# Performance work log

Measured on AMD Instinct MI355X. Metric: run time of the kernel, lower is better.

## Reference

```python
import jax, jax.numpy as jnp
import numpy as np
import math

D_MODEL = 1024
N_HEADS = 16
D_HEAD = D_MODEL // N_HEADS
D_FF = 4096
BATCH = 2
SEQ = 2048
EPS = 1e-5


def _rmsnorm(x, w):
    rms = jnp.sqrt(jnp.mean(x * x, axis=-1, keepdims=True) + EPS)
    return (x / rms) * w


def _gelu_erf(x):
    # matches 0.5 * x * (1 + erf(x / sqrt(2)))
    return 0.5 * x * (1.0 + jax.lax.erf(x / jnp.sqrt(jnp.asarray(2.0, x.dtype))))


def setup_inputs() -> dict:
    key = jax.random.key(0)
    ks = jax.random.split(key, 6)
    scale = 0.02
    x = jax.random.normal(ks[0], (BATCH, SEQ, D_MODEL), dtype=jnp.float32)
    w_qkv = jax.random.normal(ks[1], (3 * D_MODEL, D_MODEL), dtype=jnp.float32) * scale
    w_o = jax.random.normal(ks[2], (D_MODEL, D_MODEL), dtype=jnp.float32) * scale
    ln1_w = jnp.ones((D_MODEL,), dtype=jnp.float32)
    ln2_w = jnp.ones((D_MODEL,), dtype=jnp.float32)
    w1 = jax.random.normal(ks[3], (D_FF, D_MODEL), dtype=jnp.float32) * scale
    w2 = jax.random.normal(ks[4], (D_MODEL, D_FF), dtype=jnp.float32) * scale
    return {"x": x, "w_qkv": w_qkv, "w_o": w_o, "ln1_w": ln1_w,
            "ln2_w": ln2_w, "w1": w1, "w2": w2}


def reference(x, w_qkv, w_o, ln1_w, ln2_w, w1, w2):
    B, S, D = x.shape
    # --- attention sublayer (pre-norm) ---
    h = _rmsnorm(x, ln1_w)
    qkv = jnp.einsum('bsd,ed->bse', h, w_qkv)            # (B,S,3*D)
    qkv = qkv.reshape(B, S, 3, N_HEADS, D_HEAD)
    q, k, v = jnp.moveaxis(qkv, 2, 0)                    # each (B,S,H,dh)
    q = q.transpose(0, 2, 1, 3)                          # (B,H,S,dh)
    k = k.transpose(0, 2, 1, 3)
    v = v.transpose(0, 2, 1, 3)
    scores = jnp.einsum('bhqd,bhkd->bhqk', q, k) / math.sqrt(D_HEAD)
    causal = jnp.tril(jnp.ones((S, S), dtype=bool))      # True = keep
    scores = jnp.where(causal, scores, jnp.asarray(-jnp.inf, scores.dtype))
    attn = jax.nn.softmax(scores, axis=-1)
    ctx = jnp.einsum('bhqk,bhkd->bhqd', attn, v)         # (B,H,S,dh)
    ctx = ctx.transpose(0, 2, 1, 3).reshape(B, S, D)
    attn_out = jnp.einsum('bsd,ed->bse', ctx, w_o)
    first_sum = x + attn_out
    # --- FFN sublayer (pre-norm) ---
    h2 = _rmsnorm(first_sum, ln2_w)
    ff = jnp.einsum('bsf,df->bsd', _gelu_erf(jnp.einsum('bsd,fd->bsf', h2, w1)), w2)
    return first_sum + ff
```

## Files before the change

kernel.cpp:

```cpp
#include <hip/hip_runtime.h>

typedef unsigned short u16;
typedef unsigned int u32;
typedef __attribute__((ext_vector_type(8))) short short8;
typedef __attribute__((ext_vector_type(4))) float f32x4;

#define AS1 __attribute__((address_space(1)))
#define AS3 __attribute__((address_space(3)))

__device__ __forceinline__ u16 f2bf(float f) {
  union { float f; unsigned u; } v; v.f = f;
  return (u16)((v.u + 0x7fffu + ((v.u >> 16) & 1u)) >> 16);
}
__device__ __forceinline__ u32 pack2bf(float a, float b) {
  return (u32)f2bf(a) | ((u32)f2bf(b) << 16);
}
__device__ __forceinline__ float bf2f(u16 h) {
  union { u32 u; float f; } v; v.u = ((u32)h) << 16; return v.f;
}
__device__ __forceinline__ u32 permpack(float a, float b) {
  union { float f; u32 u; } ua, ub; ua.f = a; ub.f = b;
  return __builtin_amdgcn_perm(ub.u, ua.u, 0x07060302u);
}


__global__ __launch_bounds__(256)
void packb_kernel(const float* __restrict__ wqkv, const float* __restrict__ wo,
                  const float* __restrict__ w1, const float* __restrict__ w2,
                  u16* __restrict__ oqkv, u16* __restrict__ oo,
                  u16* __restrict__ o1, u16* __restrict__ o2) {
  __shared__ u16 Ls[128][40];
  const int b = blockIdx.x, t = threadIdx.x;
  const float* W; u16* O; int nb, kb, KB; float scale = 1.0f;
  if (b < 768)       { W = wqkv; O = oqkv; KB = 32;  int i2 = b;        nb = i2 >> 5; kb = i2 & 31;
                       if (nb >= 8 && nb < 16) scale = 0.125f; }
  else if (b < 1024) { W = wo;   O = oo;   KB = 32;  int i2 = b - 768;  nb = i2 >> 5; kb = i2 & 31; }
  else if (b < 2048) { W = w1;   O = o1;   KB = 32;  int i2 = b - 1024; nb = i2 >> 5; kb = i2 & 31; }
  else               { W = w2;   O = o2;   KB = 128; int i2 = b - 2048; nb = i2 >> 7; kb = i2 & 127; }
  const int K = KB * 32;
  {
    const int r = t >> 1, c0 = (t & 1) * 16;
    const float* src = W + (size_t)(nb * 128 + r) * K + kb * 32 + c0;
#pragma unroll
    for (int e = 0; e < 16; ++e) Ls[r][c0 + e] = f2bf(src[e] * scale);
  }
  __syncthreads();
  const int f = t >> 5, l0 = (t & 31) * 2;
  u16* dst = O + ((size_t)(nb * KB + kb) * 8 + f) * 512 + (size_t)l0 * 8;
  short8 v0, v1;
#pragma unroll
  for (int e = 0; e < 8; ++e) v0[e] = (short)Ls[f * 16 + (l0 & 15)][(l0 >> 4) * 8 + e];
  const int l1 = l0 + 1;
#pragma unroll
  for (int e = 0; e < 8; ++e) v1[e] = (short)Ls[f * 16 + (l1 & 15)][(l1 >> 4) * 8 + e];
  *(short8*)dst = v0;
  *(short8*)(dst + 8) = v1;
}

__global__ void rmsnorm_kernel(const float* __restrict__ x, const float* __restrict__ w,
                               u16* __restrict__ out) {
  const int row = blockIdx.x, tid = threadIdx.x;
  const float4 v = ((const float4*)(x + (size_t)row * 1024))[tid];
  float ss = v.x * v.x + v.y * v.y + v.z * v.z + v.w * v.w;
#pragma unroll
  for (int off = 32; off > 0; off >>= 1) ss += __shfl_xor(ss, off);
  __shared__ float red[4];
  if ((tid & 63) == 0) red[tid >> 6] = ss;
  __syncthreads();
  float tot = red[0] + red[1] + red[2] + red[3];
  float scale = 1.0f / sqrtf(tot * (1.0f / 1024.0f) + 1e-5f);
  const float4 wv = ((const float4*)w)[tid];
  const int kb = tid >> 3, quadp = (tid >> 1) & 3, e0 = (tid & 1) * 4;
  const int mb = row >> 7, i_o = (row >> 4) & 7, l16_o = row & 15;
  size_t off = (((size_t)mb * 32 + kb) * 8 + i_o) * 512 + (quadp * 16 + l16_o) * 8 + e0;
  u32 lo = pack2bf(v.x * scale * wv.x, v.y * scale * wv.y);
  u32 hi = pack2bf(v.z * scale * wv.z, v.w * scale * wv.w);
  *(uint2*)(out + off) = make_uint2(lo, hi);
}

template <int EPI>
__global__ __launch_bounds__(256, 3)
void gemm_pp(const u16* __restrict__ Ap, const u16* __restrict__ Bp,
             const float* __restrict__ RES, void* __restrict__ OUT,
             int M, int N, int K, int KS) {
  __shared__ __align__(16) u16 As[2][4096];
  const int tid = threadIdx.x;
  const int wave = tid >> 6, lane = tid & 63;
  const int quad = lane >> 4, l16 = lane & 15;
  int bx = blockIdx.x, by = blockIdx.y;
  const int gx = gridDim.x, gy = gridDim.y;
  if (((gx & 1) | (gy & 3)) == 0) {
    const int lin = blockIdx.x + gx * blockIdx.y;
    const int xcd = lin & 7, j = lin >> 3;
    const int rw = gx >> 1;
    bx = (xcd & 1) * rw + j % rw;
    by = (xcd >> 1) * (gy >> 2) + j / rw;
  }
  const int wm = (wave >> 1) * 64, wn = (wave & 1) * 64;
  const int KB = K >> 5;
  f32x4 acc[4][4] = {};

  const int kb0 = (blockIdx.z * KS) >> 5;
  const int nit = KS >> 5;
  const u16* Ag = Ap + ((size_t)by * KB + kb0) * 4096 + wave * 1024 + lane * 8;
  const u16* Bw = Bp + (((size_t)bx * KB + kb0) * 8 + (wn >> 4)) * 512 + (size_t)lane * 8;

  auto stage = [&](int it, int pp) {
    const u16* s = Ag + (size_t)it * 4096;
    u16* d = &As[pp][wave * 1024];
    __builtin_amdgcn_global_load_lds((AS1 void*)s, (AS3 void*)d, 16, 0, 0);
    __builtin_amdgcn_global_load_lds((AS1 void*)(s + 512), (AS3 void*)(d + 512), 16, 0, 0);
  };

  stage(0, 0);
  short8 bfr[4];
#pragma unroll
  for (int j = 0; j < 4; ++j) bfr[j] = *(const short8*)(Bw + j * 512);
  int p = 0;
  const int abase = (wm >> 4) * 512;
  for (int it = 0; it < nit - 1; ++it) {
    __syncthreads();
    stage(it + 1, p ^ 1);
    short8 bn[4];
    {
      const u16* bp = Bw + (size_t)(it + 1) * 4096;
#pragma unroll
      for (int j = 0; j < 4; ++j) bn[j] = *(const short8*)(bp + j * 512);
    }
    short8 af[4];
#pragma unroll
    for (int i = 0; i < 4; ++i)
      af[i] = *(const short8*)(&As[p][abase + i * 512 + lane * 8]);
#pragma unroll
    for (int i = 0; i < 4; ++i)
#pragma unroll
      for (int j = 0; j < 4; ++j)
        acc[i][j] = __builtin_amdgcn_mfma_f32_16x16x32_bf16(af[i], bfr[j], acc[i][j], 0, 0, 0);
#pragma unroll
    for (int j = 0; j < 4; ++j) bfr[j] = bn[j];
    p ^= 1;
  }
  {
    __syncthreads();
    short8 af[4];
#pragma unroll
    for (int i = 0; i < 4; ++i)
      af[i] = *(const short8*)(&As[p][abase + i * 512 + lane * 8]);
#pragma unroll
    for (int i = 0; i < 4; ++i)
#pragma unroll
      for (int j = 0; j < 4; ++j)
        acc[i][j] = __builtin_amdgcn_mfma_f32_16x16x32_bf16(af[i], bfr[j], acc[i][j], 0, 0, 0);
  }

  const int m0 = by * 128, n0 = bx * 128;
  const size_t zoff = (size_t)blockIdx.z * M * N;
#pragma unroll
  for (int i = 0; i < 4; ++i) {
#pragma unroll
    for (int j = 0; j < 4; ++j) {
#pragma unroll
      for (int r = 0; r < 4; ++r) {
        int row = m0 + wm + i * 16 + quad * 4 + r;
        int col = n0 + wn + j * 16 + l16;
        size_t idx = (size_t)row * N + col;
        float v = acc[i][j][r];
        if constexpr (EPI == 0) {
          ((u16*)OUT)[idx] = f2bf(v);
        } else if constexpr (EPI == 1) {
          ((float*)OUT)[idx] = RES[idx] + v;
        } else if constexpr (EPI == 2) {
          float g = 0.5f * v * (1.0f + erff(v * 0.70710678118654752f));
          const int kb_o = col >> 5, quadp = (col >> 3) & 3, e = col & 7;
          const int mb_o = row >> 7, i_o = (row >> 4) & 7, l16_o = row & 15;
          size_t off = (((size_t)mb_o * (N >> 5) + kb_o) * 8 + i_o) * 512
                       + (quadp * 16 + l16_o) * 8 + e;
          ((u16*)OUT)[off] = f2bf(g);
        } else {
          ((u16*)OUT)[zoff + idx] = f2bf(v);
        }
      }
    }
  }
}

__global__ void reduce4_kernel(const float* __restrict__ fs,
                               const u16* __restrict__ P,
                               float* __restrict__ out, size_t n) {
  size_t i = ((size_t)blockIdx.x * 256 + threadIdx.x) * 4;
  float4 a = *(const float4*)(fs + i);
  float s[4] = {a.x, a.y, a.z, a.w};
#pragma unroll
  for (int z = 0; z < 4; ++z) {
    ushort4 q = *(const ushort4*)(P + z * n + i);
    s[0] += bf2f(q.x); s[1] += bf2f(q.y); s[2] += bf2f(q.z); s[3] += bf2f(q.w);
  }
  *(float4*)(out + i) = make_float4(s[0], s[1], s[2], s[3]);
}

__global__ __launch_bounds__(256)
void packkv_kernel(const u16* __restrict__ qkv, u16* __restrict__ Kp,
                   u16* __restrict__ Vp) {
  __shared__ __align__(16) u16 Ks[32][72];
  __shared__ __align__(16) u16 Vs[32][72];
  const int kt = blockIdx.x, h = blockIdx.y, b = blockIdx.z;
  const int tid = threadIdx.x;
  const int key0 = kt * 32;
  {
    const size_t g = (size_t)b * 2048 * 3072 + (size_t)(key0 + (tid >> 3)) * 3072
                     + h * 64 + (tid & 7) * 8;
    *(short8*)(&Ks[tid >> 3][(tid & 7) * 8]) = *(const short8*)(qkv + g + 1024);
    *(short8*)(&Vs[tid >> 3][(tid & 7) * 8]) = *(const short8*)(qkv + g + 2048);
  }
  __syncthreads();
  const int wave = tid >> 6, lane = tid & 63;
  const int quad = lane >> 4, l16 = lane & 15;
  const int permrow = 8 * (l16 >> 2) + (l16 & 3);
  const size_t obase = ((size_t)((b * 16 + h) * 64 + kt)) * 2048 + tid * 8;
  {
    int row = permrow + (wave >> 1) * 4;
    int col = quad * 8 + (wave & 1) * 32;
    *(short8*)(Kp + obase) = *(const short8*)(&Ks[row][col]);
  }
  {
    short8 v;
    int col = wave * 16 + l16;
#pragma unroll
    for (int j = 0; j < 8; ++j) v[j] = (short)Vs[quad * 8 + j][col];
    *(short8*)(Vp + obase) = v;
  }
}

struct AttnState {
  f32x4 o0, o1, o2, o3;
  float ls;
};

template <bool MASKED>
__device__ __forceinline__ void attn_tile(
    AttnState& st, const u16* kp, const u16* vp, int key0, int q_abs, int quad,
    short8 qf0, short8 qf1) {
  short8 kf00 = *(const short8*)kp;
  short8 kf01 = *(const short8*)(kp + 512);
  short8 kf10 = *(const short8*)(kp + 1024);
  short8 kf11 = *(const short8*)(kp + 1536);
  short8 vf0 = *(const short8*)vp;
  short8 vf1 = *(const short8*)(vp + 512);
  short8 vf2 = *(const short8*)(vp + 1024);
  short8 vf3 = *(const short8*)(vp + 1536);

  f32x4 s0 = {}, s1 = {};
  s0 = __builtin_amdgcn_mfma_f32_16x16x32_bf16(kf00, qf0, s0, 0, 0, 0);
  s0 = __builtin_amdgcn_mfma_f32_16x16x32_bf16(kf01, qf1, s0, 0, 0, 0);
  s1 = __builtin_amdgcn_mfma_f32_16x16x32_bf16(kf10, qf0, s1, 0, 0, 0);
  s1 = __builtin_amdgcn_mfma_f32_16x16x32_bf16(kf11, qf1, s1, 0, 0, 0);

  float p[8];
#pragma unroll
  for (int r = 0; r < 4; ++r) {
    p[r]     = __expf(s0[r]);
    p[4 + r] = __expf(s1[r]);
  }
  if constexpr (MASKED) {
    const int kb = key0 + 8 * quad;
#pragma unroll
    for (int r = 0; r < 4; ++r) {
      if (kb + r > q_abs)     p[r] = 0.f;
      if (kb + 4 + r > q_abs) p[4 + r] = 0.f;
    }
  }
  st.ls += ((p[0] + p[1]) + (p[2] + p[3])) + ((p[4] + p[5]) + (p[6] + p[7]));

  union { u32 u[4]; short8 s; } pu;
  pu.u[0] = permpack(p[0], p[1]);
  pu.u[1] = permpack(p[2], p[3]);
  pu.u[2] = permpack(p[4], p[5]);
  pu.u[3] = permpack(p[6], p[7]);

  st.o0 = __builtin_amdgcn_mfma_f32_16x16x32_bf16(vf0, pu.s, st.o0, 0, 0, 0);
  st.o1 = __builtin_amdgcn_mfma_f32_16x16x32_bf16(vf1, pu.s, st.o1, 0, 0, 0);
  st.o2 = __builtin_amdgcn_mfma_f32_16x16x32_bf16(vf2, pu.s, st.o2, 0, 0, 0);
  st.o3 = __builtin_amdgcn_mfma_f32_16x16x32_bf16(vf3, pu.s, st.o3, 0, 0, 0);
}

__global__ __launch_bounds__(256)
void attn_kernel(const u16* __restrict__ qkv, const u16* __restrict__ Kpack,
                 const u16* __restrict__ Vpack, u16* __restrict__ ctx) {
  const int bx = blockIdx.x, by = blockIdx.y, bz = blockIdx.z;
  const int h = by, b = bz;
  const int qt = ((by >> 3) & 1) ? (31 - bx) : bx;
  const int tid = threadIdx.x, wave = tid >> 6, lane = tid & 63;
  const int quad = lane >> 4, l16 = lane & 15;
  const int q0 = qt * 64;
  const int qrow = q0 + wave * 16;
  const int q_abs = qrow + l16;
  const size_t base = (size_t)b * 2048 * 3072;
  const size_t headoff = (size_t)((b * 16 + h) * 64) * 2048;
  const u16* Kb = Kpack + headoff + lane * 8;
  const u16* Vb = Vpack + headoff + lane * 8;

  short8 qf0, qf1;
  {
    const u16* qp = qkv + base + (size_t)q_abs * 3072 + h * 64 + quad * 8;
    qf0 = *(const short8*)qp;
    qf1 = *(const short8*)(qp + 32);
  }
  AttnState st;
  st.o0 = f32x4{}; st.o1 = f32x4{}; st.o2 = f32x4{}; st.o3 = f32x4{};
  st.ls = 0.f;

  const int nfull = qrow >> 5;
  for (int kt = 0; kt < nfull; ++kt)
    attn_tile<false>(st, Kb + kt * 2048, Vb + kt * 2048, kt * 32, q_abs, quad, qf0, qf1);
  attn_tile<true>(st, Kb + nfull * 2048, Vb + nfull * 2048, nfull * 32, q_abs, quad, qf0, qf1);

  float ls = st.ls;
  ls += __shfl_xor(ls, 16);
  ls += __shfl_xor(ls, 32);
  float inv = 1.0f / ls;

  const int rgl = b * 2048 + q_abs;
  const int mb = rgl >> 7, i_o = (rgl >> 4) & 7;
  f32x4 o[4] = {st.o0, st.o1, st.o2, st.o3};
#pragma unroll
  for (int c = 0; c < 4; ++c) {
    const int c0 = h * 64 + c * 16 + quad * 4;
    const int kb = c0 >> 5, quadp = (c0 >> 3) & 3, e0 = c0 & 7;
    size_t off = (((size_t)mb * 32 + kb) * 8 + i_o) * 512 + (quadp * 16 + l16) * 8 + e0;
    u32 lo = pack2bf(o[c][0] * inv, o[c][1] * inv);
    u32 hi = pack2bf(o[c][2] * inv, o[c][3] * inv);
    *(uint2*)(ctx + off) = make_uint2(lo, hi);
  }
}

extern "C" void kernel_launch(void* const* d_in, const int* in_sizes, int n_in,
                              void* d_out, int out_size, void* d_ws, size_t ws_size,
                              hipStream_t stream) {
  const float* x     = (const float*)d_in[0];
  const float* w_qkv = (const float*)d_in[1];
  const float* w_o   = (const float*)d_in[2];
  const float* ln1   = (const float*)d_in[3];
  const float* ln2   = (const float*)d_in[4];
  const float* w1    = (const float*)d_in[5];
  const float* w2    = (const float*)d_in[6];
  float* out = (float*)d_out;

  char* p = (char*)d_ws;
  u16* wqkv_b = (u16*)p; p += (size_t)3072 * 1024 * 2;
  u16* wo_b   = (u16*)p; p += (size_t)1024 * 1024 * 2;
  u16* w1_b   = (u16*)p; p += (size_t)4096 * 1024 * 2;
  u16* w2_b   = (u16*)p; p += (size_t)1024 * 4096 * 2;
  u16* h_b    = (u16*)p; p += (size_t)4096 * 1024 * 2;
  u16* qkv_b  = (u16*)p;
  u16* g_b    = qkv_b;
  p += (size_t)4096 * 3072 * 2;
  u16* ctx_b  = (u16*)p; p += (size_t)4096 * 1024 * 2;
  float* fs   = (float*)p; p += (size_t)4096 * 1024 * 4;
  u16* kp_b   = (u16*)fs;
  u16* vp_b   = (u16*)fs + (size_t)4 * 1024 * 1024;
  u16* Pbuf = (u16*)p;
  const size_t need = (size_t)(p - (char*)d_ws) + (size_t)4 * 4096 * 1024 * 2;
  const bool splitk = ws_size >= need;

  packb_kernel<<<3072, 256, 0, stream>>>(w_qkv, w_o, w1, w2,
                                         wqkv_b, wo_b, w1_b, w2_b);

  rmsnorm_kernel<<<4096, 256, 0, stream>>>(x, ln1, h_b);
  gemm_pp<0><<<dim3(24, 32, 1), 256, 0, stream>>>(h_b, wqkv_b, nullptr, qkv_b, 4096, 3072, 1024, 1024);
  packkv_kernel<<<dim3(64, 16, 2), 256, 0, stream>>>(qkv_b, kp_b, vp_b);
  attn_kernel<<<dim3(32, 16, 2), 256, 0, stream>>>(qkv_b, kp_b, vp_b, ctx_b);
  gemm_pp<1><<<dim3(8, 32, 1), 256, 0, stream>>>(ctx_b, wo_b, x, fs, 4096, 1024, 1024, 1024);
  rmsnorm_kernel<<<4096, 256, 0, stream>>>(fs, ln2, h_b);
  gemm_pp<2><<<dim3(32, 32, 1), 256, 0, stream>>>(h_b, w1_b, nullptr, g_b, 4096, 4096, 1024, 1024);
  if (splitk) {
    gemm_pp<3><<<dim3(8, 32, 4), 256, 0, stream>>>(g_b, w2_b, nullptr, Pbuf, 4096, 1024, 4096, 1024);
    reduce4_kernel<<<4096, 256, 0, stream>>>(fs, Pbuf, out, (size_t)4096 * 1024);
  } else {
    gemm_pp<1><<<dim3(8, 32, 1), 256, 0, stream>>>(g_b, w2_b, fs, out, 4096, 1024, 4096, 4096);
  }
}
```

Baseline: 320.0 us.

## Split-K the output projection, unroll GEMM K-loop by two, vectorize weight packing

Several separate changes. The attention output projection GEMM now runs split-K across 4 slices into bf16 partial buffers, with a reduce kernel that adds the residual x, so a 256-block grid becomes 1024 blocks. The GEMM main loop is unrolled by two with fixed ping-pong B register sets, and launch bounds go from 3 to 4 blocks per CU. The weight packing kernel uses vectorized float4 loads and uint4 LDS stores. The risks are an extra reduce pass, partial sums rounded to bf16, and more register pressure under the higher occupancy target. The unrolled loop also assumes an even, nonzero number of K iterations.

```diff
diff --git a/kernel.cpp b/kernel.cpp
--- a/kernel.cpp
+++ b/kernel.cpp
@@ -29,7 +29,7 @@
                   const float* __restrict__ w1, const float* __restrict__ w2,
                   u16* __restrict__ oqkv, u16* __restrict__ oo,
                   u16* __restrict__ o1, u16* __restrict__ o2) {
-  __shared__ u16 Ls[128][40];
+  __shared__ __align__(16) u16 Ls[128][40];
   const int b = blockIdx.x, t = threadIdx.x;
   const float* W; u16* O; int nb, kb, KB; float scale = 1.0f;
   if (b < 768)       { W = wqkv; O = oqkv; KB = 32;  int i2 = b;        nb = i2 >> 5; kb = i2 & 31;
@@ -41,20 +41,25 @@
   {
     const int r = t >> 1, c0 = (t & 1) * 16;
     const float* src = W + (size_t)(nb * 128 + r) * K + kb * 32 + c0;
-#pragma unroll
-    for (int e = 0; e < 16; ++e) Ls[r][c0 + e] = f2bf(src[e] * scale);
-  }
-  __syncthreads();
-  const int f = t >> 5, l0 = (t & 31) * 2;
+    float4 v0 = *(const float4*)(src);
+    float4 v1 = *(const float4*)(src + 4);
+    float4 v2 = *(const float4*)(src + 8);
+    float4 v3 = *(const float4*)(src + 12);
+    uint4 a, c;
+    a.x = pack2bf(v0.x * scale, v0.y * scale); a.y = pack2bf(v0.z * scale, v0.w * scale);
+    a.z = pack2bf(v1.x * scale, v1.y * scale); a.w = pack2bf(v1.z * scale, v1.w * scale);
+    c.x = pack2bf(v2.x * scale, v2.y * scale); c.y = pack2bf(v2.z * scale, v2.w * scale);
+    c.z = pack2bf(v3.x * scale, v3.y * scale); c.w = pack2bf(v3.z * scale, v3.w * scale);
+    *(uint4*)&Ls[r][c0] = a;
+    *(uint4*)&Ls[r][c0 + 8] = c;
+  }
+  __syncthreads();
+  const int f = t >> 5, l0 = (t & 31) * 2, l1 = l0 + 1;
   u16* dst = O + ((size_t)(nb * KB + kb) * 8 + f) * 512 + (size_t)l0 * 8;
-  short8 v0, v1;
-#pragma unroll
-  for (int e = 0; e < 8; ++e) v0[e] = (short)Ls[f * 16 + (l0 & 15)][(l0 >> 4) * 8 + e];
-  const int l1 = l0 + 1;
-#pragma unroll
-  for (int e = 0; e < 8; ++e) v1[e] = (short)Ls[f * 16 + (l1 & 15)][(l1 >> 4) * 8 + e];
-  *(short8*)dst = v0;
-  *(short8*)(dst + 8) = v1;
+  uint4 w0 = *(const uint4*)&Ls[f * 16 + (l0 & 15)][(l0 >> 4) * 8];
+  uint4 w1v = *(const uint4*)&Ls[f * 16 + (l1 & 15)][(l1 >> 4) * 8];
+  *(uint4*)dst = w0;
+  *(uint4*)(dst + 8) = w1v;
 }
 
 __global__ void rmsnorm_kernel(const float* __restrict__ x, const float* __restrict__ w,
@@ -79,7 +84,7 @@
 }
 
 template <int EPI>
-__global__ __launch_bounds__(256, 3)
+__global__ __launch_bounds__(256, 4)
 void gemm_pp(const u16* __restrict__ Ap, const u16* __restrict__ Bp,
              const float* __restrict__ RES, void* __restrict__ OUT,
              int M, int N, int K, int KS) {
@@ -111,47 +116,43 @@
     __builtin_amdgcn_global_load_lds((AS1 void*)s, (AS3 void*)d, 16, 0, 0);
     __builtin_amdgcn_global_load_lds((AS1 void*)(s + 512), (AS3 void*)(d + 512), 16, 0, 0);
   };
-
-  stage(0, 0);
-  short8 bfr[4];
-#pragma unroll
-  for (int j = 0; j < 4; ++j) bfr[j] = *(const short8*)(Bw + j * 512);
-  int p = 0;
+  auto loadB = [&](short8* dst, int it) {
+    const u16* bp = Bw + (size_t)it * 4096;
+#pragma unroll
+    for (int j = 0; j < 4; ++j) dst[j] = *(const short8*)(bp + j * 512);
+  };
   const int abase = (wm >> 4) * 512;
-  for (int it = 0; it < nit - 1; ++it) {
-    __syncthreads();
-    stage(it + 1, p ^ 1);
-    short8 bn[4];
-    {
-      const u16* bp = Bw + (size_t)(it + 1) * 4096;
-#pragma unroll
-      for (int j = 0; j < 4; ++j) bn[j] = *(const short8*)(bp + j * 512);
-    }
+  auto compute = [&](int pp, const short8* bfr) {
     short8 af[4];
 #pragma unroll
     for (int i = 0; i < 4; ++i)
-      af[i] = *(const short8*)(&As[p][abase + i * 512 + lane * 8]);
+      af[i] = *(const short8*)(&As[pp][abase + i * 512 + lane * 8]);
 #pragma unroll
     for (int i = 0; i < 4; ++i)
 #pragma unroll
       for (int j = 0; j < 4; ++j)
         acc[i][j] = __builtin_amdgcn_mfma_f32_16x16x32_bf16(af[i], bfr[j], acc[i][j], 0, 0, 0);
-#pragma unroll
-    for (int j = 0; j < 4; ++j) bfr[j] = bn[j];
-    p ^= 1;
-  }
-  {
+  };
+
+  short8 b0[4], b1[4];
+  stage(0, 0);
+  loadB(b0, 0);
+  for (int it = 0; it + 2 < nit; it += 2) {
     __syncthreads();
-    short8 af[4];
-#pragma unroll
-    for (int i = 0; i < 4; ++i)
-      af[i] = *(const short8*)(&As[p][abase + i * 512 + lane * 8]);
-#pragma unroll
-    for (int i = 0; i < 4; ++i)
-#pragma unroll
-      for (int j = 0; j < 4; ++j)
-        acc[i][j] = __builtin_amdgcn_mfma_f32_16x16x32_bf16(af[i], bfr[j], acc[i][j], 0, 0, 0);
-  }
+    stage(it + 1, 1);
+    loadB(b1, it + 1);
+    compute(0, b0);
+    __syncthreads();
+    stage(it + 2, 0);
+    loadB(b0, it + 2);
+    compute(1, b1);
+  }
+  __syncthreads();
+  stage(nit - 1, 1);
+  loadB(b1, nit - 1);
+  compute(0, b0);
+  __syncthreads();
+  compute(1, b1);
 
   const int m0 = by * 128, n0 = bx * 128;
   const size_t zoff = (size_t)blockIdx.z * M * N;
@@ -184,11 +185,11 @@
   }
 }
 
-__global__ void reduce4_kernel(const float* __restrict__ fs,
+__global__ void reduce4_kernel(const float* __restrict__ base,
                                const u16* __restrict__ P,
                                float* __restrict__ out, size_t n) {
   size_t i = ((size_t)blockIdx.x * 256 + threadIdx.x) * 4;
-  float4 a = *(const float4*)(fs + i);
+  float4 a = *(const float4*)(base + i);
   float s[4] = {a.x, a.y, a.z, a.w};
 #pragma unroll
   for (int z = 0; z < 4; ++z) {
@@ -369,7 +370,12 @@
   gemm_pp<0><<<dim3(24, 32, 1), 256, 0, stream>>>(h_b, wqkv_b, nullptr, qkv_b, 4096, 3072, 1024, 1024);
   packkv_kernel<<<dim3(64, 16, 2), 256, 0, stream>>>(qkv_b, kp_b, vp_b);
   attn_kernel<<<dim3(32, 16, 2), 256, 0, stream>>>(qkv_b, kp_b, vp_b, ctx_b);
-  gemm_pp<1><<<dim3(8, 32, 1), 256, 0, stream>>>(ctx_b, wo_b, x, fs, 4096, 1024, 1024, 1024);
+  if (splitk) {
+    gemm_pp<3><<<dim3(8, 32, 4), 256, 0, stream>>>(ctx_b, wo_b, nullptr, Pbuf, 4096, 1024, 1024, 256);
+    reduce4_kernel<<<4096, 256, 0, stream>>>(x, Pbuf, fs, (size_t)4096 * 1024);
+  } else {
+    gemm_pp<1><<<dim3(8, 32, 1), 256, 0, stream>>>(ctx_b, wo_b, x, fs, 4096, 1024, 1024, 1024);
+  }
   rmsnorm_kernel<<<4096, 256, 0, stream>>>(fs, ln2, h_b);
   gemm_pp<2><<<dim3(32, 32, 1), 256, 0, stream>>>(h_b, w1_b, nullptr, g_b, 4096, 4096, 1024, 1024);
   if (splitk) {
```

Result: slower. 327.3 us (+2.3%).
